# Performance work log

Measured on AMD Instinct MI355X. Metric: run time of the kernel, lower is better.

Reference implementation:

```python
import jax, jax.numpy as jnp
from jax import lax
import numpy as np

ROI = 7  # roi_size


def _extract_rois(feat, coords):
    """Faithful port of extract_roi_features: clamp a 7x7 window to image bounds,
    then bilinearly resize the (possibly smaller) crop back to 7x7
    (F.interpolate, mode='bilinear', align_corners=False)."""
    B, C, H, W = feat.shape
    half = ROI // 2

    def axis_idx(c, size):
        start = jnp.maximum(0, c - half)                  # [B,A]
        end = jnp.minimum(size, c + half + 1)
        Li = end - start                                  # crop length (int) [B,A]
        L = Li.astype(feat.dtype)[..., None]              # [B,A,1]
        j = jnp.arange(ROI, dtype=feat.dtype)
        # align_corners=False source coordinate, clamped into the crop
        src = jnp.clip((j + 0.5) * L / ROI - 0.5, 0.0, L - 1.0)  # [B,A,7]
        i0 = jnp.floor(src).astype(jnp.int32)
        i1 = jnp.minimum(i0 + 1, Li[..., None] - 1)
        w1 = src - i0.astype(feat.dtype)
        return start[..., None] + i0, start[..., None] + i1, 1.0 - w1, w1

    xc = coords[..., 0].astype(jnp.int32)
    yc = coords[..., 1].astype(jnp.int32)
    y0, y1, wy0, wy1 = axis_idx(yc, H)
    x0, x1, wx0, wx1 = axis_idx(xc, W)
    Bn, A = xc.shape
    bi = jnp.arange(Bn)[:, None, None, None]

    def g(Y, X):  # gather -> [B,A,7,7,C]
        return feat[bi, :, Y[:, :, :, None], X[:, :, None, :]]

    wy0 = wy0[:, :, :, None, None]; wy1 = wy1[:, :, :, None, None]
    wx0 = wx0[:, :, None, :, None]; wx1 = wx1[:, :, None, :, None]
    v = (wy0 * wx0 * g(y0, x0) + wy0 * wx1 * g(y0, x1)
         + wy1 * wx0 * g(y1, x0) + wy1 * wx1 * g(y1, x1))
    return jnp.transpose(v, (0, 1, 4, 2, 3))  # [B,A,C,7,7]


def _conv(x, w, b, pad):
    y = lax.conv_general_dilated(x, w, (1, 1), [(pad, pad), (pad, pad)],
                                 dimension_numbers=('NCHW', 'OIHW', 'NCHW'))
    return y + b[None, :, None, None]


def _bn(x, scale, bias, mean, var, eps=1e-5):
    inv = scale * lax.rsqrt(var + eps)
    return x * inv[None, :, None, None] + (bias - mean * inv)[None, :, None, None]


def setup_inputs() -> dict:
    key = jax.random.key(0)
    ks = jax.random.split(key, 12)
    B, A, C, H, W = 8, 128, 256, 64, 64
    f32 = jnp.float32
    d = {}
    d['feat_rgb'] = jax.random.normal(ks[0], (B, C, H, W), f32)
    d['feat_tir'] = jax.random.normal(ks[1], (B, C, H, W), f32)
    d['anchor_coords'] = jax.random.randint(ks[2], (B, A, 2), 0, 64).astype(jnp.int32)
    # local_fusion: Conv(2C->C,3) BN ReLU Conv(C->C,3) BN ReLU
    d['conv1_w'] = jax.random.normal(ks[3], (C, 2 * C, 3, 3), f32) * 0.02
    d['conv1_b'] = jnp.zeros((C,), f32)
    d['bn1_scale'] = jnp.ones((C,), f32)
    d['bn1_bias'] = jnp.zeros((C,), f32)
    d['bn1_mean'] = jax.random.normal(ks[4], (C,), f32) * 0.1
    d['bn1_var'] = jax.random.uniform(ks[5], (C,), f32, 0.5, 1.5)
    d['conv2_w'] = jax.random.normal(ks[6], (C, C, 3, 3), f32) * 0.02
    d['conv2_b'] = jnp.zeros((C,), f32)
    d['bn2_scale'] = jnp.ones((C,), f32)
    d['bn2_bias'] = jnp.zeros((C,), f32)
    d['bn2_mean'] = jax.random.normal(ks[7], (C,), f32) * 0.1
    d['bn2_var'] = jax.random.uniform(ks[8], (C,), f32, 0.5, 1.5)
    # weight_generator: Conv(C->C//4,1) ReLU Conv(C//4->2,1) Softmax(dim=1)
    d['wg1_w'] = jax.random.normal(ks[9], (C // 4, C, 1, 1), f32) * 0.05
    d['wg1_b'] = jnp.zeros((C // 4,), f32)
    d['wg2_w'] = jax.random.normal(ks[10], (2, C // 4, 1, 1), f32) * 0.05
    d['wg2_b'] = jnp.zeros((2,), f32)
    return d


def reference(feat_rgb, feat_tir, anchor_coords,
              conv1_w, conv1_b, bn1_scale, bn1_bias, bn1_mean, bn1_var,
              conv2_w, conv2_b, bn2_scale, bn2_bias, bn2_mean, bn2_var,
              wg1_w, wg1_b, wg2_w, wg2_b):
    B, C, H, W = feat_rgb.shape
    A = anchor_coords.shape[1]
    roi_rgb = _extract_rois(feat_rgb, anchor_coords)  # [B,A,C,7,7]
    roi_tir = _extract_rois(feat_tir, anchor_coords)
    rgb = roi_rgb.reshape(B * A, C, ROI, ROI)
    tir = roi_tir.reshape(B * A, C, ROI, ROI)
    x = jnp.concatenate([rgb, tir], axis=1)           # [B*A, 2C, 7, 7]
    x = jax.nn.relu(_bn(_conv(x, conv1_w, conv1_b, 1), bn1_scale, bn1_bias, bn1_mean, bn1_var))
    x = jax.nn.relu(_bn(_conv(x, conv2_w, conv2_b, 1), bn2_scale, bn2_bias, bn2_mean, bn2_var))
    h = jax.nn.relu(_conv(x, wg1_w, wg1_b, 0))
    w = jax.nn.softmax(_conv(h, wg2_w, wg2_b, 0), axis=1)  # [B*A, 2, 7, 7]
    fused = w[:, 0:1] * rgb + w[:, 1:2] * tir
    return fused.reshape(B, A, C, ROI, ROI)
```

## Files before the change

### kernel.cpp

```cpp
#include <hip/hip_runtime.h>
#include <cstddef>
#include <cstdint>


typedef unsigned int u32;
typedef unsigned short u16;
typedef __attribute__((ext_vector_type(8))) short short8;
typedef __attribute__((ext_vector_type(4))) float float4v;

__device__ __forceinline__ float bf2f(u16 u) {
  u32 x = ((u32)u) << 16;
  return __builtin_bit_cast(float, x);
}
__device__ __forceinline__ u16 f2bf(float f) {
  u32 x = __builtin_bit_cast(u32, f);
  x = x + 0x7fffu + ((x >> 16) & 1u);
  return (u16)(x >> 16);
}
__device__ __forceinline__ void gl_lds16(const void* g, void* l) {
  __builtin_amdgcn_global_load_lds((const __attribute__((address_space(1))) void*)g,
                                   (__attribute__((address_space(3))) void*)l, 16, 0, 0);
}

template <int IC>
__global__ void k_prep_w(const float* __restrict__ w, u16* __restrict__ wt) {
  int i = blockIdx.x * 256 + threadIdx.x;
  if (i >= 9 * 256 * IC) return;
  int t = i / (256 * IC);
  int rem = i - t * 256 * IC;
  int oc = rem / IC, ic = rem - oc * IC;
  wt[i] = f2bf(w[((size_t)oc * IC + ic) * 9 + t]);
}

__global__ void k_prep_bn(const float* __restrict__ cb, const float* __restrict__ sc,
                          const float* __restrict__ bi, const float* __restrict__ mn,
                          const float* __restrict__ vr, float* __restrict__ sb) {
  int c = threadIdx.x;
  float inv = sc[c] * rsqrtf(vr[c] + 1e-5f);
  sb[c]       = inv;
  sb[256 + c] = cb[c] * inv + (bi[c] - mn[c] * inv);
}

__global__ __launch_bounds__(256)
void k_roi2(const float* __restrict__ frgb, const float* __restrict__ ftir,
            const int* __restrict__ coords, u16* __restrict__ cat) {
  int ba = blockIdx.x, b = ba >> 7, tid = threadIdx.x;
  __shared__ int   si0[2][7], si1[2][7];
  __shared__ float sw0[2][7], sw1[2][7];
  __shared__ u16 tile[49][514];
  if (tid < 14) {
    int axis = tid / 7;
    int j = tid - axis * 7;
    int c = coords[ba * 2 + (axis == 0 ? 1 : 0)];
    int start = max(0, c - 3);
    int end   = min(64, c + 4);
    int Li = end - start;
    float L = (float)Li;
    float src = ((float)j + 0.5f) * L / 7.0f - 0.5f;
    src = fminf(fmaxf(src, 0.0f), L - 1.0f);
    int i0 = (int)floorf(src);
    int i1 = min(i0 + 1, Li - 1);
    float w1 = src - (float)i0;
    si0[axis][j] = start + i0;
    si1[axis][j] = start + i1;
    sw0[axis][j] = 1.0f - w1;
    sw1[axis][j] = w1;
  }
  __syncthreads();
  const float* fr = frgb + (size_t)b * 256 * 4096;
  const float* ft = ftir + (size_t)b * 256 * 4096;
  for (int idx = tid; idx < 256 * 49; idx += 256) {
    int c = idx / 49, p = idx - c * 49;
    int jy = p / 7, jx = p - (p / 7) * 7;
    int y0 = si0[0][jy], y1 = si1[0][jy];
    int x0 = si0[1][jx], x1 = si1[1][jx];
    float wy0 = sw0[0][jy], wy1 = sw1[0][jy];
    float wx0 = sw0[1][jx], wx1 = sw1[1][jx];
    float a00 = wy0 * wx0, a01 = wy0 * wx1, a10 = wy1 * wx0, a11 = wy1 * wx1;
    const float* fc = fr + (size_t)c * 4096;
    float vr_ = a00 * fc[y0 * 64 + x0] + a01 * fc[y0 * 64 + x1] +
                a10 * fc[y1 * 64 + x0] + a11 * fc[y1 * 64 + x1];
    const float* gc = ft + (size_t)c * 4096;
    float vt_ = a00 * gc[y0 * 64 + x0] + a01 * gc[y0 * 64 + x1] +
                a10 * gc[y1 * 64 + x0] + a11 * gc[y1 * 64 + x1];
    tile[p][c]       = f2bf(vr_);
    tile[p][256 + c] = f2bf(vt_);
  }
  __syncthreads();
  u16* dst = cat + (size_t)ba * 81 * 512;
  for (int o = tid; o < 81 * 512; o += 256) {
    int row = o >> 9, c = o & 511;
    int py0 = row / 9, px0 = row - (row / 9) * 9;
    u16 v = 0;
    if (py0 >= 1 && py0 <= 7 && px0 >= 1 && px0 <= 7)
      v = tile[(py0 - 1) * 7 + (px0 - 1)][c];
    dst[o] = v;
  }
}

template <int ICT, bool FIRST>
__global__ __launch_bounds__(256, 2)
void k_conv_mfma(const u16* __restrict__ IN, const u16* __restrict__ WT,
                 const float* __restrict__ sb, u16* __restrict__ OUT) {
  constexpr int NC = ICT / 64;
  constexpr int BUFB = 2 * 81 * 128;
  __shared__ __align__(16) u16 lds[2][BUFB / 2];
  const int tid = threadIdx.x;
  const int lane = tid & 63, wv = tid >> 6;
  const int l15 = lane & 15, hi = lane >> 4;
  const int ba2 = blockIdx.x * 2;
  const char* inb = (const char*)IN;

  if (FIRST) {
#pragma unroll
    for (int i = 0; i < 32; ++i) {
      int row = (i < 9) ? i : (i < 18) ? (63 + i)
                                       : (9 * ((i - 18) / 2 + 1) + ((i - 18) & 1) * 8);
      OUT[((size_t)ba2 * 81 + row) * 256 + tid] = 0;
      OUT[((size_t)(ba2 + 1) * 81 + row) * 256 + tid] = 0;
    }
  }

  int rg[7];
  {
    int lp = (l15 < 14) ? l15 : (l15 - 14);
#pragma unroll
    for (int pf = 0; pf < 7; ++pf) {
      int P = 14 * pf + lp;
      int roi = (P >= 49) ? 1 : 0;
      int q = P - roi * 49;
      rg[pf] = roi * 81 + (q / 7) * 9 + (q - (q / 7) * 7);
    }
  }

  float4v acc[7][4];
#pragma unroll
  for (int a = 0; a < 7; ++a)
#pragma unroll
    for (int f = 0; f < 4; ++f) acc[a][f] = (float4v){0.f, 0.f, 0.f, 0.f};

  auto stage = [&](int ch, int buf) {
    for (int s = wv; s < 21; s += 4) {
      int d = s * 1024 + lane * 16;
      if (d < BUFB) {
        int u = d ^ (((d >> 7) & 7) << 4);
        int row_g = u >> 7;
        int col = u & 127;
        int roi = (row_g >= 81) ? 1 : 0;
        int rr = row_g - roi * 81;
        const char* src = inb + ((size_t)(ba2 + roi) * 81 + rr) * (ICT * 2) +
                          ch * 128 + col;
        gl_lds16(src, (char*)&lds[buf][0] + s * 1024);
      }
    }
  };

  stage(0, 0);
  __syncthreads();

  const u16* wthr = WT + ((size_t)(wv * 64 + l15)) * ICT + hi * 8;

  int cur = 0;
#pragma unroll 1
  for (int ch = 0; ch < NC; ++ch) {
    if (ch + 1 < NC) stage(ch + 1, cur ^ 1);
    const char* lb = (const char*)&lds[cur][0];
    const int chk = ch * 64;
    short8 wfr[2][4];
#pragma unroll
    for (int f = 0; f < 4; ++f)
      wfr[0][f] = *(const short8*)(wthr + (size_t)(f * 16) * ICT + chk);
#pragma unroll
    for (int j = 0; j < 18; ++j) {
      const int t = j >> 1, kk = j & 1;
      const int dy = t / 3, dx = t - (t / 3) * 3;
      if (j < 17) {
        const int t2 = (j + 1) >> 1, k2 = (j + 1) & 1;
#pragma unroll
        for (int f = 0; f < 4; ++f)
          wfr[(j + 1) & 1][f] =
              *(const short8*)(wthr + (size_t)(t2 * 256 + f * 16) * ICT + chk + k2 * 32);
      }
      short8 bfr[7];
#pragma unroll
      for (int pf = 0; pf < 7; ++pf) {
        int rr = rg[pf] + dy * 9 + dx;
        int byt = (rr * 128 + kk * 64 + hi * 16) ^ ((rr & 7) << 4);
        bfr[pf] = *(const short8*)(lb + byt);
      }
      __builtin_amdgcn_s_setprio(1);
#pragma unroll
      for (int pf = 0; pf < 7; ++pf)
#pragma unroll
        for (int f = 0; f < 4; ++f)
          acc[pf][f] = FIRST
              ? __builtin_amdgcn_mfma_f32_16x16x32_bf16(bfr[pf], wfr[j & 1][f],
                                                        acc[pf][f], 0, 0, 0)
              : __builtin_amdgcn_mfma_f32_16x16x32_bf16(wfr[j & 1][f], bfr[pf],
                                                        acc[pf][f], 0, 0, 0);
      __builtin_amdgcn_s_setprio(0);
    }
    __syncthreads();
    cur ^= 1;
  }

  if (FIRST) {
    u16* ob = OUT + (size_t)ba2 * 81 * 256;
#pragma unroll
    for (int f = 0; f < 4; ++f) {
      int oc = wv * 64 + f * 16 + l15;
      float s = sb[oc], bb = sb[256 + oc];
#pragma unroll
      for (int pf = 0; pf < 7; ++pf)
#pragma unroll
        for (int reg = 0; reg < 4; ++reg) {
          int r = hi * 4 + reg;
          if (r < 14) {
            int P = 14 * pf + r;
            int roi = (P >= 49) ? 1 : 0;
            int q = P - roi * 49;
            int pp = (q / 7 + 1) * 9 + (q - (q / 7) * 7) + 1;
            ob[((size_t)roi * 81 + pp) * 256 + oc] =
                f2bf(fmaxf(acc[pf][f][reg] * s + bb, 0.0f));
          }
        }
    }
  } else {
    u16* ob = OUT + (size_t)ba2 * 256 * 49;
    if (l15 < 14) {
#pragma unroll
      for (int f = 0; f < 4; ++f)
#pragma unroll
        for (int reg = 0; reg < 4; ++reg) {
          int oc = wv * 64 + f * 16 + hi * 4 + reg;
          float s = sb[oc], bb = sb[256 + oc];
#pragma unroll
          for (int pf = 0; pf < 7; ++pf) {
            int P = 14 * pf + l15;
            int roi = (P >= 49) ? 1 : 0;
            int q = P - roi * 49;
            ob[((size_t)roi * 256 + oc) * 49 + q] =
                f2bf(fmaxf(acc[pf][f][reg] * s + bb, 0.0f));
          }
        }
    }
  }
}

__global__ __launch_bounds__(256)
void k_head_fuse(const u16* __restrict__ x3, const u16* __restrict__ cat,
                 const float* __restrict__ w1, const float* __restrict__ b1,
                 const float* __restrict__ w2, const float* __restrict__ b2,
                 float* __restrict__ out) {
  int ba  = blockIdx.x;
  int tid = threadIdx.x;
  __shared__ float xs[256 * 49];
  __shared__ float hs[64 * 49];
  __shared__ float ls[2 * 49];
  __shared__ float swx[2 * 49];
  const u16* src = x3 + (size_t)ba * 256 * 49;
  for (int idx = tid; idx < 256 * 49; idx += 256) xs[idx] = bf2f(src[idx]);
  __syncthreads();
  for (int idx = tid; idx < 64 * 49; idx += 256) {
    int oh = idx / 49, p = idx - oh * 49;
    float s = b1[oh];
    const float* wr = w1 + oh * 256;
    for (int ic = 0; ic < 256; ++ic) s += wr[ic] * xs[ic * 49 + p];
    hs[idx] = fmaxf(s, 0.0f);
  }
  __syncthreads();
  if (tid < 98) {
    int chn = tid / 49, p = tid - chn * 49;
    float s = b2[chn];
    const float* wr = w2 + chn * 64;
    for (int k = 0; k < 64; ++k) s += wr[k] * hs[k * 49 + p];
    ls[tid] = s;
  }
  __syncthreads();
  if (tid < 49) {
    float l0 = ls[tid], l1 = ls[49 + tid];
    float m = fmaxf(l0, l1);
    float e0 = expf(l0 - m), e1 = expf(l1 - m);
    float d = e0 + e1;
    swx[tid]      = e0 / d;
    swx[49 + tid] = e1 / d;
  }
  __syncthreads();
  const u16* cr = cat + (size_t)ba * 81 * 512;
  float* o = out + (size_t)ba * 256 * 49;
  for (int idx = tid; idx < 256 * 49; idx += 256) {
    int c = idx / 49, p = idx - (idx / 49) * 49;
    int pp = (p / 7 + 1) * 9 + (p - (p / 7) * 7) + 1;
    float rgb = bf2f(cr[pp * 512 + c]);
    float tir = bf2f(cr[pp * 512 + 256 + c]);
    o[idx] = swx[p] * rgb + swx[49 + p] * tir;
  }
}

extern "C" void kernel_launch(void* const* d_in, const int* in_sizes, int n_in,
                              void* d_out, int out_size, void* d_ws, size_t ws_size,
                              hipStream_t stream) {
  const float* feat_rgb = (const float*)d_in[0];
  const float* feat_tir = (const float*)d_in[1];
  const int*   coords   = (const int*)d_in[2];
  const float* conv1_w  = (const float*)d_in[3];
  const float* conv1_b  = (const float*)d_in[4];
  const float* bn1_s    = (const float*)d_in[5];
  const float* bn1_b    = (const float*)d_in[6];
  const float* bn1_m    = (const float*)d_in[7];
  const float* bn1_v    = (const float*)d_in[8];
  const float* conv2_w  = (const float*)d_in[9];
  const float* conv2_b  = (const float*)d_in[10];
  const float* bn2_s    = (const float*)d_in[11];
  const float* bn2_b    = (const float*)d_in[12];
  const float* bn2_m    = (const float*)d_in[13];
  const float* bn2_v    = (const float*)d_in[14];
  const float* wg1_w    = (const float*)d_in[15];
  const float* wg1_b    = (const float*)d_in[16];
  const float* wg2_w    = (const float*)d_in[17];
  const float* wg2_b    = (const float*)d_in[18];
  float* out = (float*)d_out;

  char* base = (char*)d_ws;
  u16*   W1T  = (u16*)(base);
  u16*   W2T  = (u16*)(base + 2359296);
  float* SB1  = (float*)(base + 2359296 + 1179648);
  float* SB2  = (float*)(base + 2359296 + 1179648 + 2048);
  u16*   CAT2 = (u16*)(base + 2359296 + 1179648 + 4096);
  u16*   X2   = (u16*)(base + 2359296 + 1179648 + 4096 + 84934656);
  u16*   X3   = (u16*)(base + 2359296 + 1179648 + 4096 + 84934656 + 42467328);

  k_prep_w<512><<<(9 * 256 * 512 + 255) / 256, 256, 0, stream>>>(conv1_w, W1T);
  k_prep_w<256><<<(9 * 256 * 256 + 255) / 256, 256, 0, stream>>>(conv2_w, W2T);
  k_prep_bn<<<1, 256, 0, stream>>>(conv1_b, bn1_s, bn1_b, bn1_m, bn1_v, SB1);
  k_prep_bn<<<1, 256, 0, stream>>>(conv2_b, bn2_s, bn2_b, bn2_m, bn2_v, SB2);
  k_roi2<<<1024, 256, 0, stream>>>(feat_rgb, feat_tir, coords, CAT2);
  k_conv_mfma<512, true><<<512, 256, 0, stream>>>(CAT2, W1T, SB1, X2);
  k_conv_mfma<256, false><<<512, 256, 0, stream>>>(X2, W2T, SB2, X3);
  k_head_fuse<<<1024, 256, 0, stream>>>(X3, CAT2, wg1_w, wg1_b, wg2_w, wg2_b, out);
}
```

Before: 620.2 us.

## Split conv MFMA work across 8 waves by pixel groups

Both conv kernels now run with 512 threads per block. The 8 waves form a 4x2 grid: 4 output-channel groups and 2 pixel-fragment groups. Each wave holds 4 (or 3) pixel fragments instead of 7, which lowers accumulator register pressure and doubles the waves available to hide LDS and global latency. The cost is that every weight fragment is now loaded by twice as many waves, and the pixel fragments are split unevenly (4 vs 3) between the two groups.

Measured after the change: 834.5 us. +34.6%, slower.

```diff
diff --git a/kernel.cpp b/kernel.cpp
--- a/kernel.cpp
+++ b/kernel.cpp
@@ -99,7 +99,7 @@
 }
 
 template <int ICT, bool FIRST>
-__global__ __launch_bounds__(256, 2)
+__global__ __launch_bounds__(512, 4)
 void k_conv_mfma(const u16* __restrict__ IN, const u16* __restrict__ WT,
                  const float* __restrict__ sb, u16* __restrict__ OUT) {
   constexpr int NC = ICT / 64;
@@ -107,40 +107,44 @@
   __shared__ __align__(16) u16 lds[2][BUFB / 2];
   const int tid = threadIdx.x;
   const int lane = tid & 63, wv = tid >> 6;
+  const int ng = wv & 3, mg = wv >> 2;
   const int l15 = lane & 15, hi = lane >> 4;
   const int ba2 = blockIdx.x * 2;
   const char* inb = (const char*)IN;
 
   if (FIRST) {
+    int oc = tid & 255, rh = tid >> 8;
+    u16* ob = OUT + ((size_t)(ba2 + rh) * 81) * 256 + oc;
 #pragma unroll
     for (int i = 0; i < 32; ++i) {
       int row = (i < 9) ? i : (i < 18) ? (63 + i)
                                        : (9 * ((i - 18) / 2 + 1) + ((i - 18) & 1) * 8);
-      OUT[((size_t)ba2 * 81 + row) * 256 + tid] = 0;
-      OUT[((size_t)(ba2 + 1) * 81 + row) * 256 + tid] = 0;
-    }
-  }
-
-  int rg[7];
+      ob[row * 256] = 0;
+    }
+  }
+
+  int rg[4];
   {
     int lp = (l15 < 14) ? l15 : (l15 - 14);
 #pragma unroll
-    for (int pf = 0; pf < 7; ++pf) {
-      int P = 14 * pf + lp;
+    for (int pfl = 0; pfl < 4; ++pfl) {
+      int pfg = 2 * pfl + mg;
+      if (pfg > 6) pfg = 0;
+      int P = 14 * pfg + lp;
       int roi = (P >= 49) ? 1 : 0;
       int q = P - roi * 49;
-      rg[pf] = roi * 81 + (q / 7) * 9 + (q - (q / 7) * 7);
-    }
-  }
-
-  float4v acc[7][4];
-#pragma unroll
-  for (int a = 0; a < 7; ++a)
+      rg[pfl] = roi * 81 + (q / 7) * 9 + (q - (q / 7) * 7);
+    }
+  }
+
+  float4v acc[4][4];
+#pragma unroll
+  for (int a = 0; a < 4; ++a)
 #pragma unroll
     for (int f = 0; f < 4; ++f) acc[a][f] = (float4v){0.f, 0.f, 0.f, 0.f};
 
   auto stage = [&](int ch, int buf) {
-    for (int s = wv; s < 21; s += 4) {
+    for (int s = wv; s < 21; s += 8) {
       int d = s * 1024 + lane * 16;
       if (d < BUFB) {
         int u = d ^ (((d >> 7) & 7) << 4);
@@ -158,7 +162,7 @@
   stage(0, 0);
   __syncthreads();
 
-  const u16* wthr = WT + ((size_t)(wv * 64 + l15)) * ICT + hi * 8;
+  const u16* wthr = WT + ((size_t)(ng * 64 + l15)) * ICT + hi * 8;
 
   int cur = 0;
 #pragma unroll 1
@@ -181,23 +185,26 @@
           wfr[(j + 1) & 1][f] =
               *(const short8*)(wthr + (size_t)(t2 * 256 + f * 16) * ICT + chk + k2 * 32);
       }
-      short8 bfr[7];
-#pragma unroll
-      for (int pf = 0; pf < 7; ++pf) {
-        int rr = rg[pf] + dy * 9 + dx;
+      short8 bfr[4];
+#pragma unroll
+      for (int pfl = 0; pfl < 4; ++pfl) {
+        if (pfl == 3 && mg != 0) continue;
+        int rr = rg[pfl] + dy * 9 + dx;
         int byt = (rr * 128 + kk * 64 + hi * 16) ^ ((rr & 7) << 4);
-        bfr[pf] = *(const short8*)(lb + byt);
+        bfr[pfl] = *(const short8*)(lb + byt);
       }
       __builtin_amdgcn_s_setprio(1);
 #pragma unroll
-      for (int pf = 0; pf < 7; ++pf)
+      for (int pfl = 0; pfl < 4; ++pfl) {
+        if (pfl == 3 && mg != 0) continue;
 #pragma unroll
         for (int f = 0; f < 4; ++f)
-          acc[pf][f] = FIRST
-              ? __builtin_amdgcn_mfma_f32_16x16x32_bf16(bfr[pf], wfr[j & 1][f],
-                                                        acc[pf][f], 0, 0, 0)
-              : __builtin_amdgcn_mfma_f32_16x16x32_bf16(wfr[j & 1][f], bfr[pf],
-                                                        acc[pf][f], 0, 0, 0);
+          acc[pfl][f] = FIRST
+              ? __builtin_amdgcn_mfma_f32_16x16x32_bf16(bfr[pfl], wfr[j & 1][f],
+                                                        acc[pfl][f], 0, 0, 0)
+              : __builtin_amdgcn_mfma_f32_16x16x32_bf16(wfr[j & 1][f], bfr[pfl],
+                                                        acc[pfl][f], 0, 0, 0);
+      }
       __builtin_amdgcn_s_setprio(0);
     }
     __syncthreads();
@@ -208,22 +215,25 @@
     u16* ob = OUT + (size_t)ba2 * 81 * 256;
 #pragma unroll
     for (int f = 0; f < 4; ++f) {
-      int oc = wv * 64 + f * 16 + l15;
+      int oc = ng * 64 + f * 16 + l15;
       float s = sb[oc], bb = sb[256 + oc];
 #pragma unroll
-      for (int pf = 0; pf < 7; ++pf)
+      for (int pfl = 0; pfl < 4; ++pfl) {
+        if (pfl == 3 && mg != 0) continue;
+        int pfg = 2 * pfl + mg;
 #pragma unroll
         for (int reg = 0; reg < 4; ++reg) {
           int r = hi * 4 + reg;
           if (r < 14) {
-            int P = 14 * pf + r;
+            int P = 14 * pfg + r;
             int roi = (P >= 49) ? 1 : 0;
             int q = P - roi * 49;
             int pp = (q / 7 + 1) * 9 + (q - (q / 7) * 7) + 1;
             ob[((size_t)roi * 81 + pp) * 256 + oc] =
-                f2bf(fmaxf(acc[pf][f][reg] * s + bb, 0.0f));
+                f2bf(fmaxf(acc[pfl][f][reg] * s + bb, 0.0f));
           }
         }
+      }
     }
   } else {
     u16* ob = OUT + (size_t)ba2 * 256 * 49;
@@ -232,15 +242,17 @@
       for (int f = 0; f < 4; ++f)
 #pragma unroll
         for (int reg = 0; reg < 4; ++reg) {
-          int oc = wv * 64 + f * 16 + hi * 4 + reg;
+          int oc = ng * 64 + f * 16 + hi * 4 + reg;
           float s = sb[oc], bb = sb[256 + oc];
 #pragma unroll
-          for (int pf = 0; pf < 7; ++pf) {
-            int P = 14 * pf + l15;
+          for (int pfl = 0; pfl < 4; ++pfl) {
+            if (pfl == 3 && mg != 0) continue;
+            int pfg = 2 * pfl + mg;
+            int P = 14 * pfg + l15;
             int roi = (P >= 49) ? 1 : 0;
             int q = P - roi * 49;
             ob[((size_t)roi * 256 + oc) * 49 + q] =
-                f2bf(fmaxf(acc[pf][f][reg] * s + bb, 0.0f));
+                f2bf(fmaxf(acc[pfl][f][reg] * s + bb, 0.0f));
           }
         }
     }
@@ -335,7 +347,7 @@
   k_prep_bn<<<1, 256, 0, stream>>>(conv1_b, bn1_s, bn1_b, bn1_m, bn1_v, SB1);
   k_prep_bn<<<1, 256, 0, stream>>>(conv2_b, bn2_s, bn2_b, bn2_m, bn2_v, SB2);
   k_roi2<<<1024, 256, 0, stream>>>(feat_rgb, feat_tir, coords, CAT2);
-  k_conv_mfma<512, true><<<512, 256, 0, stream>>>(CAT2, W1T, SB1, X2);
-  k_conv_mfma<256, false><<<512, 256, 0, stream>>>(X2, W2T, SB2, X3);
+  k_conv_mfma<512, true><<<512, 512, 0, stream>>>(CAT2, W1T, SB1, X2);
+  k_conv_mfma<256, false><<<512, 512, 0, stream>>>(X2, W2T, SB2, X3);
   k_head_fuse<<<1024, 256, 0, stream>>>(X3, CAT2, wg1_w, wg1_b, wg2_w, wg2_b, out);
 }
```
